# Performance work log

Hardware: AMD Instinct MI355X
Metric: run time of the kernel (lower is better)

Reference implementation:

```python
import jax, jax.numpy as jnp
import numpy as np

PI = np.pi
B, T, L = 1024, 16, 16
XDIM = T * L * 2  # 512
H = 1024
NSTEPS = 10
EPS = 0.1
BETA = 4.0


def convert_to_angle(x):
    # wrap to [-pi, pi)
    return jnp.mod(x + PI, 2.0 * PI) - PI


def setup_inputs() -> dict:
    key = jax.random.key(0)
    ks = jax.random.split(key, 32)
    inp = {
        'x': jax.random.uniform(ks[0], (B, XDIM), jnp.float32, -PI, PI),
        'v': jax.random.normal(ks[1], (2, B, XDIM), jnp.float32),
        'eps': jnp.full((1,), EPS, jnp.float32),
        'beta': jnp.full((1,), BETA, jnp.float32),
        'rand_dir': jax.random.uniform(ks[2], (B,), jnp.float32),
        'rand_accept': jax.random.uniform(ks[3], (B,), jnp.float32),
        'masks': ((jnp.arange(XDIM)[None, :] % 2) == (jnp.arange(NSTEPS)[:, None] % 2)).astype(jnp.float32),
    }
    names = ['W1', 'b1', 'W2', 'b2', 'Ws', 'bs', 'Wt', 'bt', 'Wq', 'bq']
    shapes = [(2 * XDIM, H), (H,), (H, H), (H,), (H, XDIM), (XDIM,), (H, XDIM), (XDIM,), (H, XDIM), (XDIM,)]
    i = 4
    for pre in ['x', 'v']:
        for n, s in zip(names, shapes):
            inp[pre + n] = 0.02 * jax.random.normal(ks[i], s, jnp.float32)
            i += 1
    return inp


def _net(inp, W1, b1, W2, b2, Ws, bs, Wt, bt, Wq, bq):
    h = jnp.tanh(inp @ W1 + b1)
    h = jnp.tanh(h @ W2 + b2)
    S = jnp.tanh(h @ Ws + bs)   # scale
    Tt = h @ Wt + bt            # translation
    Q = jnp.tanh(h @ Wq + bq)   # transformation
    return S, Tt, Q


def _apply_transition(x, v, eps, beta, rand_dir, rand_accept, masks, xparams, vparams):
    eps = eps[0]
    beta_s = beta[0]

    def plaq_sums(xx):
        xl = xx.reshape(-1, T, L, 2)
        return (xl[..., 0] - xl[..., 1]
                - jnp.roll(xl[..., 0], shift=-1, axis=2)
                + jnp.roll(xl[..., 1], shift=-1, axis=1))

    def action(xx):  # [B]
        return beta_s * jnp.sum(1.0 - jnp.cos(plaq_sums(xx)), axis=(1, 2))

    grad_action = jax.grad(lambda xx: jnp.sum(action(xx)))

    def vnet(xx, g):
        return _net(jnp.concatenate([xx, g], axis=-1), *vparams)

    def xnet(vv, mx):
        return _net(jnp.concatenate([vv, mx], axis=-1), *xparams)

    def update_v_fwd(xx, vv, ld):
        g = grad_action(xx)
        S, Tt, Q = vnet(xx, g)
        sc = 0.5 * eps * S
        vv = vv * jnp.exp(sc) - 0.5 * eps * (g * jnp.exp(eps * Q) + Tt)
        return vv, ld + jnp.sum(sc, axis=1)

    def update_x_fwd(xx, vv, m, ld):
        mb = 1.0 - m
        S, Tt, Q = xnet(vv, m * xx)
        sc = eps * S
        xnew = m * xx + mb * (xx * jnp.exp(sc) + eps * (vv * jnp.exp(eps * Q) + Tt))
        return convert_to_angle(xnew), ld + jnp.sum(mb * sc, axis=1)

    def fwd_step(carry, m):
        xx, vv, ld = carry
        vv, ld = update_v_fwd(xx, vv, ld)
        xx, ld = update_x_fwd(xx, vv, m, ld)
        xx, ld = update_x_fwd(xx, vv, 1.0 - m, ld)
        vv, ld = update_v_fwd(xx, vv, ld)
        return (xx, vv, ld), None

    def update_v_bwd(xx, vv, ld):
        g = grad_action(xx)
        S, Tt, Q = vnet(xx, g)
        sc = -0.5 * eps * S
        vv = jnp.exp(sc) * (vv + 0.5 * eps * (g * jnp.exp(eps * Q) + Tt))
        return vv, ld + jnp.sum(sc, axis=1)

    def update_x_bwd(xx, vv, m, ld):
        mb = 1.0 - m
        S, Tt, Q = xnet(vv, m * xx)
        sc = -eps * S
        xnew = m * xx + mb * jnp.exp(sc) * (xx - eps * (vv * jnp.exp(eps * Q) + Tt))
        return convert_to_angle(xnew), ld + jnp.sum(mb * sc, axis=1)

    def bwd_step(carry, m):
        xx, vv, ld = carry
        vv, ld = update_v_bwd(xx, vv, ld)
        xx, ld = update_x_bwd(xx, vv, 1.0 - m, ld)  # invert forward's 2nd x-update first
        xx, ld = update_x_bwd(xx, vv, m, ld)
        vv, ld = update_v_bwd(xx, vv, ld)
        return (xx, vv, ld), None

    zero = jnp.zeros(x.shape[0], x.dtype)
    (xf, vf, ldf), _ = jax.lax.scan(fwd_step, (x, v[0], zero), masks)
    (xb, vb, ldb), _ = jax.lax.scan(bwd_step, (x, v[1], zero), jnp.flip(masks, 0))

    mf = (rand_dir < 0.5).astype(x.dtype)
    mb_ = 1.0 - mf
    v_init = v[0] * mf[:, None] + v[1] * mb_[:, None]
    x_prop = xf * mf[:, None] + xb * mb_[:, None]
    v_prop = vf * mf[:, None] + vb * mb_[:, None]
    sld_prop = ldf * mf + ldb * mb_

    h_init = action(x) + 0.5 * jnp.sum(v_init ** 2, axis=1)
    h_prop = action(x_prop) + 0.5 * jnp.sum(v_prop ** 2, axis=1)
    px = jnp.exp(jnp.minimum(h_init - h_prop + sld_prop, 0.0))

    ma = (rand_accept < px).astype(x.dtype)
    x_out = convert_to_angle(ma[:, None] * x_prop + (1.0 - ma)[:, None] * x)
    sld_out = ma * sld_prop
    return x_out, px, sld_out


def reference(x, v, eps, beta, rand_dir, rand_accept, masks,
              xW1, xb1, xW2, xb2, xWs, xbs, xWt, xbt, xWq, xbq,
              vW1, vb1, vW2, vb2, vWs, vbs, vWt, vbt, vWq, vbq):
    xparams = (xW1, xb1, xW2, xb2, xWs, xbs, xWt, xbt, xWq, xbq)
    vparams = (vW1, vb1, vW2, vb2, vWs, vbs, vWt, vbt, vWq, vbq)
    return _apply_transition(x, v, eps, beta, rand_dir, rand_accept, masks, xparams, vparams)
```

## Files before the change

### kernel.cpp

```cpp
#include <hip/hip_runtime.h>
#include <math.h>

namespace {

constexpr int NB = 1024;
constexpr int ND = 512;
constexpr int NH = 1024;
constexpr int NM = 2048;
constexpr int KTOT = 1024;

typedef __attribute__((ext_vector_type(8))) short short8;
typedef __attribute__((ext_vector_type(4))) float floatx4;

__device__ __forceinline__ unsigned short f2bf(float f) {
  unsigned int u = __float_as_uint(f);
  unsigned int r = (u + 0x7FFFu + ((u >> 16) & 1u)) >> 16;
  return (unsigned short)r;
}
__device__ __forceinline__ float bf2f(unsigned short h) {
  return __uint_as_float(((unsigned int)h) << 16);
}
__device__ __forceinline__ void split2(float f, unsigned short& h, unsigned short& l) {
  h = f2bf(f);
  l = f2bf(f - bf2f(h));
}

__device__ __forceinline__ float wrap_angle(float x) {
  const float PI_F = 3.14159265358979323846f;
  const float TWO_PI = 6.28318530717958647692f;
  const float INV_TWO_PI = 0.15915494309189533577f;
  float y = x + PI_F;
  float r = y - TWO_PI * floorf(y * INV_TWO_PI);
  return r - PI_F;
}

__device__ __forceinline__ void gload16(const void* g, void* l) {
  __builtin_amdgcn_global_load_lds(
      (const __attribute__((address_space(1))) void*)g,
      (__attribute__((address_space(3))) void*)l, 16, 0, 0);
}

__global__ __launch_bounds__(256) void tcvt_k(
    const float* __restrict__ in, int N,
    unsigned short* __restrict__ out_hi, unsigned short* __restrict__ out_lo,
    int rowoff)
{
  __shared__ float t[32][33];
  int tx = threadIdx.x, ty = threadIdx.y;
  int k0 = blockIdx.y * 32, n0 = blockIdx.x * 32;
#pragma unroll
  for (int i = 0; i < 4; ++i)
    t[ty * 4 + i][tx] = in[(size_t)(k0 + ty * 4 + i) * N + n0 + tx];
  __syncthreads();
#pragma unroll
  for (int i = 0; i < 4; ++i) {
    float f = t[tx][ty * 4 + i];
    unsigned short h, l;
    split2(f, h, l);
    size_t idx = (size_t)(rowoff + n0 + ty * 4 + i) * KTOT + k0 + tx;
    out_hi[idx] = h;
    out_lo[idx] = l;
  }
}

template <int ACT, int OUTF32>
__global__ __launch_bounds__(256) void gemm_k(
    const unsigned short* __restrict__ A0h, const unsigned short* __restrict__ A0l,
    const unsigned short* __restrict__ A1h, const unsigned short* __restrict__ A1l,
    int sA,
    const unsigned short* __restrict__ Bh, const unsigned short* __restrict__ Bl,
    const float* __restrict__ bias,
    float* __restrict__ outf,
    unsigned short* __restrict__ oh, unsigned short* __restrict__ ol,
    int ldo, int NBN)
{
  __shared__ __align__(16) unsigned short As_h[4][64 * 32];
  __shared__ __align__(16) unsigned short As_l[4][64 * 32];
  __shared__ __align__(16) unsigned short Bs_h[4][64 * 32];
  __shared__ __align__(16) unsigned short Bs_l[4][64 * 32];

  const int tid = threadIdx.x, lane = tid & 63, w = tid >> 6;

  const int bid = blockIdx.x;
  const int xcd = bid & 7, idx = bid >> 3;
  const int mb = (xcd & 3) * 8 + (idx & 7);
  const int nb = (xcd >> 2) * (NBN >> 1) + (idx >> 3);
  const int row0 = mb * 64, col0 = nb * 64;

  const int lrow = lane >> 2, lslot = lane & 3;
  const int rl = w * 16 + lrow;
  const int kg = lslot ^ ((rl >> 1) & 3);
  const int aoff = (row0 + rl) * sA + kg * 8;
  const int boff = (col0 + rl) * KTOT + kg * 8;
  const int ldsOff = w * 512 + lane * 8;

  auto stage = [&](int buf, int kk) {
    int koff = (kk & 15) * 32;
    const unsigned short* ah = (kk >= 16) ? A1h : A0h;
    const unsigned short* al = (kk >= 16) ? A1l : A0l;
    gload16(ah + aoff + koff, &As_h[buf][ldsOff]);
    gload16(al + aoff + koff, &As_l[buf][ldsOff]);
    gload16(Bh + boff + kk * 32, &Bs_h[buf][ldsOff]);
    gload16(Bl + boff + kk * 32, &Bs_l[buf][ldsOff]);
  };

  const int wr = w >> 1, wc = w & 1;
  const int rsel = lane & 15, ksel = lane >> 4;
  int aro[2], bro[2];
#pragma unroll
  for (int i = 0; i < 2; ++i) {
    int ra = wr * 32 + i * 16 + rsel;
    aro[i] = ra * 32 + ((ksel ^ ((ra >> 1) & 3)) * 8);
    int rb = wc * 32 + i * 16 + rsel;
    bro[i] = rb * 32 + ((ksel ^ ((rb >> 1) & 3)) * 8);
  }

  floatx4 acc[2][2];
#pragma unroll
  for (int i = 0; i < 2; ++i)
#pragma unroll
    for (int j = 0; j < 2; ++j) acc[i][j] = (floatx4)0.f;

  stage(0, 0);
  stage(1, 1);
  stage(2, 2);

#pragma unroll 4
  for (int kt = 0; kt < 32; ++kt) {
    const int buf = kt & 3;
    if (kt <= 29)      asm volatile("s_waitcnt vmcnt(8)" ::: "memory");
    else if (kt == 30) asm volatile("s_waitcnt vmcnt(4)" ::: "memory");
    else               asm volatile("s_waitcnt vmcnt(0)" ::: "memory");
    __builtin_amdgcn_s_barrier();
    __builtin_amdgcn_sched_barrier(0);
    if (kt < 29) stage((kt + 3) & 3, kt + 3);
    short8 ah8[2], al8[2], bh8[2], bl8[2];
#pragma unroll
    for (int i = 0; i < 2; ++i) {
      ah8[i] = *reinterpret_cast<const short8*>(&As_h[buf][aro[i]]);
      al8[i] = *reinterpret_cast<const short8*>(&As_l[buf][aro[i]]);
      bh8[i] = *reinterpret_cast<const short8*>(&Bs_h[buf][bro[i]]);
      bl8[i] = *reinterpret_cast<const short8*>(&Bs_l[buf][bro[i]]);
    }
    __builtin_amdgcn_s_setprio(1);
#pragma unroll
    for (int i = 0; i < 2; ++i)
#pragma unroll
      for (int j = 0; j < 2; ++j) {
        acc[i][j] = __builtin_amdgcn_mfma_f32_16x16x32_bf16(
            ah8[i], bh8[j], acc[i][j], 0, 0, 0);
        acc[i][j] = __builtin_amdgcn_mfma_f32_16x16x32_bf16(
            ah8[i], bl8[j], acc[i][j], 0, 0, 0);
        acc[i][j] = __builtin_amdgcn_mfma_f32_16x16x32_bf16(
            al8[i], bh8[j], acc[i][j], 0, 0, 0);
      }
    __builtin_amdgcn_s_setprio(0);
  }

#pragma unroll
  for (int i = 0; i < 2; ++i)
#pragma unroll
    for (int j = 0; j < 2; ++j) {
      int gr = row0 + wr * 32 + i * 16 + ksel * 4;
      int gc = col0 + wc * 32 + j * 16 + rsel;
      float bb = bias[gc];
      bool dt = (ACT == 1) || (ACT == 2 && !(gc >= 512 && gc < 1024));
#pragma unroll
      for (int rg = 0; rg < 4; ++rg) {
        float v = acc[i][j][rg] + bb;
        if (dt) v = tanhf(v);
        if constexpr (OUTF32) {
          outf[(size_t)(gr + rg) * ldo + gc] = v;
        } else {
          unsigned short h, l;
          split2(v, h, l);
          oh[(size_t)(gr + rg) * ldo + gc] = h;
          ol[(size_t)(gr + rg) * ldo + gc] = l;
        }
      }
    }
}

__device__ __forceinline__ void grad_from_lds(
    const float* xsh, float* sp, float beta, int row,
    float* __restrict__ g, unsigned short* __restrict__ gh,
    unsigned short* __restrict__ gl)
{
  int s0 = threadIdx.x * 2;
#pragma unroll
  for (int u = 0; u < 2; ++u) {
    int s = s0 + u, tt = s >> 4, l = s & 15;
    float p = xsh[s * 2] - xsh[s * 2 + 1]
            - xsh[(tt * 16 + ((l + 1) & 15)) * 2]
            + xsh[(((tt + 1) & 15) * 16 + l) * 2 + 1];
    sp[s] = sinf(p);
  }
  __syncthreads();
  float* gr = g + (size_t)row * ND;
  unsigned short* ghr = gh + (size_t)row * ND;
  unsigned short* glr = gl + (size_t)row * ND;
#pragma unroll
  for (int u = 0; u < 2; ++u) {
    int s = s0 + u, tt = s >> 4, l = s & 15;
    float g0 = beta * (sp[s] - sp[tt * 16 + ((l - 1) & 15)]);
    float g1 = beta * (sp[((tt - 1) & 15) * 16 + l] - sp[s]);
    gr[s * 2] = g0;
    gr[s * 2 + 1] = g1;
    unsigned short h0, l0, h1v, l1v;
    split2(g0, h0, l0);
    split2(g1, h1v, l1v);
    ghr[s * 2] = h0; glr[s * 2] = l0;
    ghr[s * 2 + 1] = h1v; glr[s * 2 + 1] = l1v;
  }
}

__global__ __launch_bounds__(128) void grad_k(
    const float* __restrict__ xs, const float* __restrict__ betap,
    float* __restrict__ g, unsigned short* __restrict__ gh,
    unsigned short* __restrict__ gl)
{
  __shared__ float xsh[512];
  __shared__ float sp[256];
  int row = blockIdx.x, c = threadIdx.x << 2;
  float4 x4 = *reinterpret_cast<const float4*>(xs + (size_t)row * ND + c);
  xsh[c] = x4.x; xsh[c + 1] = x4.y; xsh[c + 2] = x4.z; xsh[c + 3] = x4.w;
  __syncthreads();
  grad_from_lds(xsh, sp, betap[0], row, g, gh, gl);
}

__global__ __launch_bounds__(128) void init_k(
    const float* __restrict__ x_in, const float* __restrict__ v_in,
    const float* __restrict__ m0F, const float* __restrict__ m0B,
    float* __restrict__ xs, float* __restrict__ vs,
    unsigned short* __restrict__ xh, unsigned short* __restrict__ xl,
    unsigned short* __restrict__ xmh, unsigned short* __restrict__ xml,
    unsigned short* __restrict__ vh, unsigned short* __restrict__ vl,
    float* __restrict__ ld)
{
  int row = blockIdx.x;
  bool fwd = row < NB;
  int c = threadIdx.x << 2;
  size_t off = (size_t)row * ND + c;
  const float* xr = x_in + (size_t)(fwd ? row : row - NB) * ND + c;
  const float* vr = v_in + off;
  const float* mk = (fwd ? m0F : m0B) + c;
  float4 x4 = *reinterpret_cast<const float4*>(xr);
  float4 v4 = *reinterpret_cast<const float4*>(vr);
  float4 m4 = *reinterpret_cast<const float4*>(mk);
  float xx[4] = {x4.x, x4.y, x4.z, x4.w};
  float vv[4] = {v4.x, v4.y, v4.z, v4.w};
  float mm[4] = {m4.x, m4.y, m4.z, m4.w};
  ushort4 xhv, xlv, xmhv, xmlv, vhv, vlv;
  unsigned short* ph = (unsigned short*)&xhv;
  unsigned short* pl = (unsigned short*)&xlv;
  unsigned short* pmh = (unsigned short*)&xmhv;
  unsigned short* pml = (unsigned short*)&xmlv;
  unsigned short* pvh = (unsigned short*)&vhv;
  unsigned short* pvl = (unsigned short*)&vlv;
#pragma unroll
  for (int j = 0; j < 4; ++j) {
    float m = fwd ? mm[j] : 1.f - mm[j];
    split2(xx[j], ph[j], pl[j]);
    split2(m * xx[j], pmh[j], pml[j]);
    split2(vv[j], pvh[j], pvl[j]);
  }
  *reinterpret_cast<float4*>(xs + off) = make_float4(xx[0], xx[1], xx[2], xx[3]);
  *reinterpret_cast<float4*>(vs + off) = make_float4(vv[0], vv[1], vv[2], vv[3]);
  *reinterpret_cast<ushort4*>(xh + off) = xhv;
  *reinterpret_cast<ushort4*>(xl + off) = xlv;
  *reinterpret_cast<ushort4*>(xmh + off) = xmhv;
  *reinterpret_cast<ushort4*>(xml + off) = xmlv;
  *reinterpret_cast<ushort4*>(vh + off) = vhv;
  *reinterpret_cast<ushort4*>(vl + off) = vlv;
  if (threadIdx.x == 0) ld[row] = 0.f;
}

__global__ __launch_bounds__(128) void upd_v_k(
    float* __restrict__ vs, const float* __restrict__ g,
    const float* __restrict__ STQ,
    const float* __restrict__ epsp, float* __restrict__ ld,
    unsigned short* __restrict__ vh, unsigned short* __restrict__ vl,
    int twice)
{
  int row = blockIdx.x;
  bool fwd = row < NB;
  int c = threadIdx.x << 2;
  float eps = epsp[0];
  size_t off = (size_t)row * ND + c;
  const float* sr = STQ + (size_t)row * 1536;
  float4 v4 = *reinterpret_cast<float4*>(vs + off);
  float4 g4 = *reinterpret_cast<const float4*>(g + off);
  float4 S4 = *reinterpret_cast<const float4*>(sr + c);
  float4 T4 = *reinterpret_cast<const float4*>(sr + 512 + c);
  float4 Q4 = *reinterpret_cast<const float4*>(sr + 1024 + c);
  float vv[4] = {v4.x, v4.y, v4.z, v4.w};
  float gg[4] = {g4.x, g4.y, g4.z, g4.w};
  float ss[4] = {S4.x, S4.y, S4.z, S4.w};
  float tt[4] = {T4.x, T4.y, T4.z, T4.w};
  float qq[4] = {Q4.x, Q4.y, Q4.z, Q4.w};
  float scsum = 0.f;
  ushort4 hv, lv;
  unsigned short* ph = (unsigned short*)&hv;
  unsigned short* pl = (unsigned short*)&lv;
#pragma unroll
  for (int j = 0; j < 4; ++j) {
    float sc = (fwd ? 0.5f : -0.5f) * eps * ss[j];
    float F = gg[j] * expf(eps * qq[j]) + tt[j];
    vv[j] = fwd ? vv[j] * expf(sc) - 0.5f * eps * F
                : expf(sc) * (vv[j] + 0.5f * eps * F);
    scsum += sc;
    if (twice) {
      vv[j] = fwd ? vv[j] * expf(sc) - 0.5f * eps * F
                  : expf(sc) * (vv[j] + 0.5f * eps * F);
      scsum += sc;
    }
    split2(vv[j], ph[j], pl[j]);
  }
  *reinterpret_cast<float4*>(vs + off) = make_float4(vv[0], vv[1], vv[2], vv[3]);
  *reinterpret_cast<ushort4*>(vh + off) = hv;
  *reinterpret_cast<ushort4*>(vl + off) = lv;
  for (int o = 32; o > 0; o >>= 1) scsum += __shfl_down(scsum, o);
  __shared__ float part[2];
  if ((threadIdx.x & 63) == 0) part[threadIdx.x >> 6] = scsum;
  __syncthreads();
  if (threadIdx.x == 0) ld[row] += part[0] + part[1];
}

__global__ __launch_bounds__(128) void upd_x_k(
    float* __restrict__ xs, const float* __restrict__ vs,
    const float* __restrict__ STQ,
    const float* __restrict__ maskF, int invF,
    const float* __restrict__ maskB, int invB,
    const float* __restrict__ nmF, int niF,
    const float* __restrict__ nmB, int niB,
    const float* __restrict__ epsp, const float* __restrict__ betap,
    float* __restrict__ g, float* __restrict__ ld,
    unsigned short* __restrict__ xh, unsigned short* __restrict__ xl,
    unsigned short* __restrict__ xmh, unsigned short* __restrict__ xml,
    unsigned short* __restrict__ gh, unsigned short* __restrict__ gl)
{
  __shared__ float xsh[512];
  __shared__ float sp[256];
  int row = blockIdx.x;
  bool fwd = row < NB;
  const float* mk = fwd ? maskF : maskB;
  const float* nmk = fwd ? nmF : nmB;
  int inv = fwd ? invF : invB;
  int ninv = fwd ? niF : niB;
  int c = threadIdx.x << 2;
  float eps = epsp[0];
  size_t off = (size_t)row * ND + c;
  const float* sr = STQ + (size_t)row * 1536;
  float4 x4 = *reinterpret_cast<float4*>(xs + off);
  float4 v4 = *reinterpret_cast<const float4*>(vs + off);
  float4 m4 = *reinterpret_cast<const float4*>(mk + c);
  float4 n4 = *reinterpret_cast<const float4*>(nmk + c);
  float4 S4 = *reinterpret_cast<const float4*>(sr + c);
  float4 T4 = *reinterpret_cast<const float4*>(sr + 512 + c);
  float4 Q4 = *reinterpret_cast<const float4*>(sr + 1024 + c);
  float xx[4] = {x4.x, x4.y, x4.z, x4.w};
  float vv[4] = {v4.x, v4.y, v4.z, v4.w};
  float mm[4] = {m4.x, m4.y, m4.z, m4.w};
  float nn[4] = {n4.x, n4.y, n4.z, n4.w};
  float ss[4] = {S4.x, S4.y, S4.z, S4.w};
  float tt[4] = {T4.x, T4.y, T4.z, T4.w};
  float qq[4] = {Q4.x, Q4.y, Q4.z, Q4.w};
  float scsum = 0.f;
  float xn[4];
  ushort4 hv, lv, mhv, mlv;
  unsigned short* ph = (unsigned short*)&hv;
  unsigned short* pl = (unsigned short*)&lv;
  unsigned short* pmh = (unsigned short*)&mhv;
  unsigned short* pml = (unsigned short*)&mlv;
#pragma unroll
  for (int j = 0; j < 4; ++j) {
    float m = inv ? 1.f - mm[j] : mm[j];
    float mb = 1.f - m;
    float es = eps * ss[j];
    float F = vv[j] * expf(eps * qq[j]) + tt[j];
    float t;
    if (fwd) {
      t = m * xx[j] + mb * (xx[j] * expf(es) + eps * F);
      scsum += mb * es;
    } else {
      t = m * xx[j] + mb * (expf(-es) * (xx[j] - eps * F));
      scsum -= mb * es;
    }
    xn[j] = wrap_angle(t);
    xsh[c + j] = xn[j];
    float nm = ninv ? 1.f - nn[j] : nn[j];
    split2(xn[j], ph[j], pl[j]);
    split2(nm * xn[j], pmh[j], pml[j]);
  }
  *reinterpret_cast<float4*>(xs + off) = make_float4(xn[0], xn[1], xn[2], xn[3]);
  *reinterpret_cast<ushort4*>(xh + off) = hv;
  *reinterpret_cast<ushort4*>(xl + off) = lv;
  *reinterpret_cast<ushort4*>(xmh + off) = mhv;
  *reinterpret_cast<ushort4*>(xml + off) = mlv;
  __syncthreads();
  grad_from_lds(xsh, sp, betap[0], row, g, gh, gl);
  for (int o = 32; o > 0; o >>= 1) scsum += __shfl_down(scsum, o);
  __shared__ float part[2];
  if ((threadIdx.x & 63) == 0) part[threadIdx.x >> 6] = scsum;
  __syncthreads();
  if (threadIdx.x == 0) ld[row] += part[0] + part[1];
}

__global__ __launch_bounds__(256) void finalize_k(
    const float* __restrict__ x_in, const float* __restrict__ v_in,
    const float* __restrict__ xs, const float* __restrict__ vs,
    const float* __restrict__ ld,
    const float* __restrict__ rdir, const float* __restrict__ racc,
    const float* __restrict__ betap,
    float* __restrict__ out_x, float* __restrict__ out_px,
    float* __restrict__ out_sld)
{
  int b = blockIdx.x, t = threadIdx.x;
  bool fwd = rdir[b] < 0.5f;
  int prow = fwd ? b : NB + b;
  const float* xp = xs + (size_t)prow * ND;
  const float* vp = vs + (size_t)prow * ND;
  const float* vi = v_in + (size_t)(fwd ? 0 : NB) * ND + (size_t)b * ND;
  float sld = ld[prow];
  __shared__ float xs0[512], xs1[512];
  const float* xr = x_in + (size_t)b * ND;
  xs0[t] = xr[t]; xs0[t + 256] = xr[t + 256];
  xs1[t] = xp[t]; xs1[t + 256] = xp[t + 256];
  __syncthreads();
  int tt = t >> 4, l = t & 15;
  int i00 = t * 2, i01 = t * 2 + 1;
  int i10 = (tt * 16 + ((l + 1) & 15)) * 2;
  int i11 = (((tt + 1) & 15) * 16 + l) * 2 + 1;
  float p0 = xs0[i00] - xs0[i01] - xs0[i10] + xs0[i11];
  float p1 = xs1[i00] - xs1[i01] - xs1[i10] + xs1[i11];
  float r0 = 1.f - cosf(p0);
  float r1 = 1.f - cosf(p1);
  float a0v = vi[t], a1v = vi[t + 256];
  float b0v = vp[t], b1v = vp[t + 256];
  float svi = a0v * a0v + a1v * a1v;
  float svp = b0v * b0v + b1v * b1v;
  for (int o = 32; o > 0; o >>= 1) {
    r0  += __shfl_down(r0, o);
    r1  += __shfl_down(r1, o);
    svi += __shfl_down(svi, o);
    svp += __shfl_down(svp, o);
  }
  __shared__ float red[4][4];
  if ((t & 63) == 0) {
    int w = t >> 6;
    red[w][0] = r0; red[w][1] = r1; red[w][2] = svi; red[w][3] = svp;
  }
  __syncthreads();
  __shared__ float px_s;
  if (t == 0) {
    float R0 = 0, R1 = 0, SI = 0, SP = 0;
    for (int w = 0; w < 4; ++w) {
      R0 += red[w][0]; R1 += red[w][1]; SI += red[w][2]; SP += red[w][3];
    }
    float beta = betap[0];
    float h_init = beta * R0 + 0.5f * SI;
    float h_prop = beta * R1 + 0.5f * SP;
    px_s = expf(fminf(h_init - h_prop + sld, 0.f));
  }
  __syncthreads();
  float px = px_s;
  bool ma = racc[b] < px;
  float* ox = out_x + (size_t)b * ND;
  ox[t]       = wrap_angle(ma ? xs1[t]       : xs0[t]);
  ox[t + 256] = wrap_angle(ma ? xs1[t + 256] : xs0[t + 256]);
  if (t == 0) {
    out_px[b] = px;
    out_sld[b] = ma ? sld : 0.f;
  }
}

}

extern "C" void kernel_launch(void* const* d_in, const int* in_sizes, int n_in,
                              void* d_out, int out_size, void* d_ws, size_t ws_size,
                              hipStream_t stream)
{
  const float* x_in = (const float*)d_in[0];
  const float* v_in = (const float*)d_in[1];
  const float* epsp = (const float*)d_in[2];
  const float* betap = (const float*)d_in[3];
  const float* rdir = (const float*)d_in[4];
  const float* racc = (const float*)d_in[5];
  const float* masks = (const float*)d_in[6];
  const float* xW1 = (const float*)d_in[7];
  const float* xb1 = (const float*)d_in[8];
  const float* xW2 = (const float*)d_in[9];
  const float* xb2 = (const float*)d_in[10];
  const float* xWs = (const float*)d_in[11];
  const float* xbs = (const float*)d_in[12];
  const float* xWt = (const float*)d_in[13];
  const float* xbt = (const float*)d_in[14];
  const float* xWq = (const float*)d_in[15];
  const float* xbq = (const float*)d_in[16];
  const float* vW1 = (const float*)d_in[17];
  const float* vb1 = (const float*)d_in[18];
  const float* vW2 = (const float*)d_in[19];
  const float* vb2 = (const float*)d_in[20];
  const float* vWs = (const float*)d_in[21];
  const float* vbs = (const float*)d_in[22];
  const float* vWt = (const float*)d_in[23];
  const float* vbt = (const float*)d_in[24];
  const float* vWq = (const float*)d_in[25];
  const float* vbq = (const float*)d_in[26];

  char* base = (char*)d_ws;
  auto alloc = [&](size_t bytes) {
    char* r = base;
    base += (bytes + 255) & ~(size_t)255;
    return r;
  };
  float* xs = (float*)alloc((size_t)NM * ND * 4);
  float* vs = (float*)alloc((size_t)NM * ND * 4);
  float* g  = (float*)alloc((size_t)NM * ND * 4);
  float* ld = (float*)alloc((size_t)NM * 4);
  unsigned short* xh  = (unsigned short*)alloc((size_t)NM * ND * 2);
  unsigned short* xl  = (unsigned short*)alloc((size_t)NM * ND * 2);
  unsigned short* xmh = (unsigned short*)alloc((size_t)NM * ND * 2);
  unsigned short* xml = (unsigned short*)alloc((size_t)NM * ND * 2);
  unsigned short* vh  = (unsigned short*)alloc((size_t)NM * ND * 2);
  unsigned short* vl  = (unsigned short*)alloc((size_t)NM * ND * 2);
  unsigned short* gh  = (unsigned short*)alloc((size_t)NM * ND * 2);
  unsigned short* gl  = (unsigned short*)alloc((size_t)NM * ND * 2);
  unsigned short* h1h = (unsigned short*)alloc((size_t)NM * NH * 2);
  unsigned short* h1l = (unsigned short*)alloc((size_t)NM * NH * 2);
  unsigned short* h2h = (unsigned short*)alloc((size_t)NM * NH * 2);
  unsigned short* h2l = (unsigned short*)alloc((size_t)NM * NH * 2);
  float* STQ = (float*)alloc((size_t)NM * 1536 * 4);
  unsigned short* xW1h = (unsigned short*)alloc((size_t)NH * KTOT * 2);
  unsigned short* xW1l = (unsigned short*)alloc((size_t)NH * KTOT * 2);
  unsigned short* xW2h = (unsigned short*)alloc((size_t)NH * KTOT * 2);
  unsigned short* xW2l = (unsigned short*)alloc((size_t)NH * KTOT * 2);
  unsigned short* xWsh = (unsigned short*)alloc((size_t)1536 * KTOT * 2);
  unsigned short* xWsl = (unsigned short*)alloc((size_t)1536 * KTOT * 2);
  unsigned short* vW1h = (unsigned short*)alloc((size_t)NH * KTOT * 2);
  unsigned short* vW1l = (unsigned short*)alloc((size_t)NH * KTOT * 2);
  unsigned short* vW2h = (unsigned short*)alloc((size_t)NH * KTOT * 2);
  unsigned short* vW2l = (unsigned short*)alloc((size_t)NH * KTOT * 2);
  unsigned short* vWsh = (unsigned short*)alloc((size_t)1536 * KTOT * 2);
  unsigned short* vWsl = (unsigned short*)alloc((size_t)1536 * KTOT * 2);
  float* bstq_x = (float*)alloc(1536 * 4);
  float* bstq_v = (float*)alloc(1536 * 4);

  dim3 tb(32, 8);
  tcvt_k<<<dim3(32, 32), tb, 0, stream>>>(xW1, 1024, xW1h, xW1l, 0);
  tcvt_k<<<dim3(32, 32), tb, 0, stream>>>(xW2, 1024, xW2h, xW2l, 0);
  tcvt_k<<<dim3(16, 32), tb, 0, stream>>>(xWs, 512, xWsh, xWsl, 0);
  tcvt_k<<<dim3(16, 32), tb, 0, stream>>>(xWt, 512, xWsh, xWsl, 512);
  tcvt_k<<<dim3(16, 32), tb, 0, stream>>>(xWq, 512, xWsh, xWsl, 1024);
  tcvt_k<<<dim3(32, 32), tb, 0, stream>>>(vW1, 1024, vW1h, vW1l, 0);
  tcvt_k<<<dim3(32, 32), tb, 0, stream>>>(vW2, 1024, vW2h, vW2l, 0);
  tcvt_k<<<dim3(16, 32), tb, 0, stream>>>(vWs, 512, vWsh, vWsl, 0);
  tcvt_k<<<dim3(16, 32), tb, 0, stream>>>(vWt, 512, vWsh, vWsl, 512);
  tcvt_k<<<dim3(16, 32), tb, 0, stream>>>(vWq, 512, vWsh, vWsl, 1024);
  hipMemcpyAsync(bstq_x,        xbs, 512 * 4, hipMemcpyDeviceToDevice, stream);
  hipMemcpyAsync(bstq_x + 512,  xbt, 512 * 4, hipMemcpyDeviceToDevice, stream);
  hipMemcpyAsync(bstq_x + 1024, xbq, 512 * 4, hipMemcpyDeviceToDevice, stream);
  hipMemcpyAsync(bstq_v,        vbs, 512 * 4, hipMemcpyDeviceToDevice, stream);
  hipMemcpyAsync(bstq_v + 512,  vbt, 512 * 4, hipMemcpyDeviceToDevice, stream);
  hipMemcpyAsync(bstq_v + 1024, vbq, 512 * 4, hipMemcpyDeviceToDevice, stream);

  init_k<<<NM, 128, 0, stream>>>(x_in, v_in, masks, masks + 9 * ND,
                                 xs, vs, xh, xl, xmh, xml, vh, vl, ld);
  grad_k<<<NM, 128, 0, stream>>>(xs, betap, g, gh, gl);

  auto vnet = [&]() {
    gemm_k<1, 0><<<512, 256, 0, stream>>>(
        xh, xl, gh, gl, 512, vW1h, vW1l, vb1, nullptr, h1h, h1l, NH, 16);
    gemm_k<1, 0><<<512, 256, 0, stream>>>(
        h1h, h1l, h1h + 512, h1l + 512, 1024, vW2h, vW2l, vb2,
        nullptr, h2h, h2l, NH, 16);
    gemm_k<2, 1><<<768, 256, 0, stream>>>(
        h2h, h2l, h2h + 512, h2l + 512, 1024, vWsh, vWsl, bstq_v,
        STQ, nullptr, nullptr, 1536, 24);
  };
  auto xnet = [&]() {
    gemm_k<1, 0><<<512, 256, 0, stream>>>(
        vh, vl, xmh, xml, 512, xW1h, xW1l, xb1, nullptr, h1h, h1l, NH, 16);
    gemm_k<1, 0><<<512, 256, 0, stream>>>(
        h1h, h1l, h1h + 512, h1l + 512, 1024, xW2h, xW2l, xb2,
        nullptr, h2h, h2l, NH, 16);
    gemm_k<2, 1><<<768, 256, 0, stream>>>(
        h2h, h2l, h2h + 512, h2l + 512, 1024, xWsh, xWsl, bstq_x,
        STQ, nullptr, nullptr, 1536, 24);
  };

  vnet();
  upd_v_k<<<NM, 128, 0, stream>>>(vs, g, STQ, epsp, ld, vh, vl, 0);
  for (int s = 0; s < 10; ++s) {
    const float* mF = masks + (size_t)s * ND;
    const float* mB = masks + (size_t)(9 - s) * ND;
    const float* mFn = masks + (size_t)((s + 1 < 10) ? s + 1 : 0) * ND;
    const float* mBn = masks + (size_t)((s + 1 < 10) ? 8 - s : 0) * ND;
    xnet();
    upd_x_k<<<NM, 128, 0, stream>>>(xs, vs, STQ, mF, 0, mB, 1, mF, 1, mB, 0,
                                    epsp, betap, g, ld,
                                    xh, xl, xmh, xml, gh, gl);
    xnet();
    upd_x_k<<<NM, 128, 0, stream>>>(xs, vs, STQ, mF, 1, mB, 0, mFn, 0, mBn, 1,
                                    epsp, betap, g, ld,
                                    xh, xl, xmh, xml, gh, gl);
    vnet();
    upd_v_k<<<NM, 128, 0, stream>>>(vs, g, STQ, epsp, ld, vh, vl,
                                    (s < 9) ? 1 : 0);
  }

  float* out_x = (float*)d_out;
  float* out_px = out_x + (size_t)NB * ND;
  float* out_sld = out_px + NB;
  finalize_k<<<NB, 256, 0, stream>>>(x_in, v_in, xs, vs, ld, rdir, racc, betap,
                                     out_x, out_px, out_sld);
}
```

Before: 2.998 ms.

## Replace LDS-staged pipelined GEMM with direct global-to-register loads

Removes the asynchronous global-to-LDS multi-buffer pipeline, the XCD-aware block index remapping and the MFMA priority hints from the split-bf16 GEMM. Each wave now reads its A and B fragments straight from global memory into registers, and a plain 2D grid is launched. This drops LDS usage and barriers, possibly raising occupancy. In exchange it loses operand sharing across waves, the overlap of memory loads with MFMA work, and L2 locality from the swizzled block order.

Measured after the change: 6.770 ms. 126% more time.

```diff
diff --git a/kernel.cpp b/kernel.cpp
--- a/kernel.cpp
+++ b/kernel.cpp
@@ -32,12 +32,6 @@
   float y = x + PI_F;
   float r = y - TWO_PI * floorf(y * INV_TWO_PI);
   return r - PI_F;
-}
-
-__device__ __forceinline__ void gload16(const void* g, void* l) {
-  __builtin_amdgcn_global_load_lds(
-      (const __attribute__((address_space(1))) void*)g,
-      (__attribute__((address_space(3))) void*)l, 16, 0, 0);
 }
 
 __global__ __launch_bounds__(256) void tcvt_k(
@@ -72,47 +66,18 @@
     const float* __restrict__ bias,
     float* __restrict__ outf,
     unsigned short* __restrict__ oh, unsigned short* __restrict__ ol,
-    int ldo, int NBN)
-{
-  __shared__ __align__(16) unsigned short As_h[4][64 * 32];
-  __shared__ __align__(16) unsigned short As_l[4][64 * 32];
-  __shared__ __align__(16) unsigned short Bs_h[4][64 * 32];
-  __shared__ __align__(16) unsigned short Bs_l[4][64 * 32];
-
+    int ldo)
+{
   const int tid = threadIdx.x, lane = tid & 63, w = tid >> 6;
-
-  const int bid = blockIdx.x;
-  const int xcd = bid & 7, idx = bid >> 3;
-  const int mb = (xcd & 3) * 8 + (idx & 7);
-  const int nb = (xcd >> 2) * (NBN >> 1) + (idx >> 3);
-  const int row0 = mb * 64, col0 = nb * 64;
-
-  const int lrow = lane >> 2, lslot = lane & 3;
-  const int rl = w * 16 + lrow;
-  const int kg = lslot ^ ((rl >> 1) & 3);
-  const int aoff = (row0 + rl) * sA + kg * 8;
-  const int boff = (col0 + rl) * KTOT + kg * 8;
-  const int ldsOff = w * 512 + lane * 8;
-
-  auto stage = [&](int buf, int kk) {
-    int koff = (kk & 15) * 32;
-    const unsigned short* ah = (kk >= 16) ? A1h : A0h;
-    const unsigned short* al = (kk >= 16) ? A1l : A0l;
-    gload16(ah + aoff + koff, &As_h[buf][ldsOff]);
-    gload16(al + aoff + koff, &As_l[buf][ldsOff]);
-    gload16(Bh + boff + kk * 32, &Bs_h[buf][ldsOff]);
-    gload16(Bl + boff + kk * 32, &Bs_l[buf][ldsOff]);
-  };
-
+  const int row0 = blockIdx.y * 64, col0 = blockIdx.x * 64;
   const int wr = w >> 1, wc = w & 1;
   const int rsel = lane & 15, ksel = lane >> 4;
-  int aro[2], bro[2];
+
+  int arow[2], brow[2];
 #pragma unroll
   for (int i = 0; i < 2; ++i) {
-    int ra = wr * 32 + i * 16 + rsel;
-    aro[i] = ra * 32 + ((ksel ^ ((ra >> 1) & 3)) * 8);
-    int rb = wc * 32 + i * 16 + rsel;
-    bro[i] = rb * 32 + ((ksel ^ ((rb >> 1) & 3)) * 8);
+    arow[i] = row0 + wr * 32 + i * 16 + rsel;
+    brow[i] = col0 + wc * 32 + i * 16 + rsel;
   }
 
   floatx4 acc[2][2];
@@ -121,28 +86,23 @@
 #pragma unroll
     for (int j = 0; j < 2; ++j) acc[i][j] = (floatx4)0.f;
 
-  stage(0, 0);
-  stage(1, 1);
-  stage(2, 2);
-
-#pragma unroll 4
+#pragma unroll 2
   for (int kt = 0; kt < 32; ++kt) {
-    const int buf = kt & 3;
-    if (kt <= 29)      asm volatile("s_waitcnt vmcnt(8)" ::: "memory");
-    else if (kt == 30) asm volatile("s_waitcnt vmcnt(4)" ::: "memory");
-    else               asm volatile("s_waitcnt vmcnt(0)" ::: "memory");
-    __builtin_amdgcn_s_barrier();
-    __builtin_amdgcn_sched_barrier(0);
-    if (kt < 29) stage((kt + 3) & 3, kt + 3);
+    const int kk = kt * 32;
+    const unsigned short* Ah = (kk >= 512) ? A1h : A0h;
+    const unsigned short* Al = (kk >= 512) ? A1l : A0l;
+    const int ka = (kk & 511) + ksel * 8;
+    const int kb = kk + ksel * 8;
     short8 ah8[2], al8[2], bh8[2], bl8[2];
 #pragma unroll
     for (int i = 0; i < 2; ++i) {
-      ah8[i] = *reinterpret_cast<const short8*>(&As_h[buf][aro[i]]);
-      al8[i] = *reinterpret_cast<const short8*>(&As_l[buf][aro[i]]);
-      bh8[i] = *reinterpret_cast<const short8*>(&Bs_h[buf][bro[i]]);
-      bl8[i] = *reinterpret_cast<const short8*>(&Bs_l[buf][bro[i]]);
+      size_t ao = (size_t)arow[i] * sA + ka;
+      ah8[i] = *reinterpret_cast<const short8*>(Ah + ao);
+      al8[i] = *reinterpret_cast<const short8*>(Al + ao);
+      size_t bo = (size_t)brow[i] * KTOT + kb;
+      bh8[i] = *reinterpret_cast<const short8*>(Bh + bo);
+      bl8[i] = *reinterpret_cast<const short8*>(Bl + bo);
     }
-    __builtin_amdgcn_s_setprio(1);
 #pragma unroll
     for (int i = 0; i < 2; ++i)
 #pragma unroll
@@ -154,7 +114,6 @@
         acc[i][j] = __builtin_amdgcn_mfma_f32_16x16x32_bf16(
             al8[i], bh8[j], acc[i][j], 0, 0, 0);
       }
-    __builtin_amdgcn_s_setprio(0);
   }
 
 #pragma unroll
@@ -569,24 +528,24 @@
   grad_k<<<NM, 128, 0, stream>>>(xs, betap, g, gh, gl);
 
   auto vnet = [&]() {
-    gemm_k<1, 0><<<512, 256, 0, stream>>>(
-        xh, xl, gh, gl, 512, vW1h, vW1l, vb1, nullptr, h1h, h1l, NH, 16);
-    gemm_k<1, 0><<<512, 256, 0, stream>>>(
+    gemm_k<1, 0><<<dim3(16, 32), 256, 0, stream>>>(
+        xh, xl, gh, gl, 512, vW1h, vW1l, vb1, nullptr, h1h, h1l, NH);
+    gemm_k<1, 0><<<dim3(16, 32), 256, 0, stream>>>(
         h1h, h1l, h1h + 512, h1l + 512, 1024, vW2h, vW2l, vb2,
-        nullptr, h2h, h2l, NH, 16);
-    gemm_k<2, 1><<<768, 256, 0, stream>>>(
+        nullptr, h2h, h2l, NH);
+    gemm_k<2, 1><<<dim3(24, 32), 256, 0, stream>>>(
         h2h, h2l, h2h + 512, h2l + 512, 1024, vWsh, vWsl, bstq_v,
-        STQ, nullptr, nullptr, 1536, 24);
+        STQ, nullptr, nullptr, 1536);
   };
   auto xnet = [&]() {
-    gemm_k<1, 0><<<512, 256, 0, stream>>>(
-        vh, vl, xmh, xml, 512, xW1h, xW1l, xb1, nullptr, h1h, h1l, NH, 16);
-    gemm_k<1, 0><<<512, 256, 0, stream>>>(
+    gemm_k<1, 0><<<dim3(16, 32), 256, 0, stream>>>(
+        vh, vl, xmh, xml, 512, xW1h, xW1l, xb1, nullptr, h1h, h1l, NH);
+    gemm_k<1, 0><<<dim3(16, 32), 256, 0, stream>>>(
         h1h, h1l, h1h + 512, h1l + 512, 1024, xW2h, xW2l, xb2,
-        nullptr, h2h, h2l, NH, 16);
-    gemm_k<2, 1><<<768, 256, 0, stream>>>(
+        nullptr, h2h, h2l, NH);
+    gemm_k<2, 1><<<dim3(24, 32), 256, 0, stream>>>(
         h2h, h2l, h2h + 512, h2l + 512, 1024, xWsh, xWsl, bstq_x,
-        STQ, nullptr, nullptr, 1536, 24);
+        STQ, nullptr, nullptr, 1536);
   };
 
   vnet();
```
